# Performance work log

Measured on AMD Instinct MI355X. Metric: run time of the kernel, lower is better.

## Reference

```python
import jax, jax.numpy as jnp
import numpy as np

B, H, M, HS = 256, 1024, 256, 128  # batch, hidden=entry_size, mem_cap, head_size
TAU = 1.0
sg = jax.lax.stop_gradient


def _gumbel(u):
    # torch: -log(1e-20 - log(1e-20 + rand))
    return -jnp.log(1e-20 - jnp.log(1e-20 + u))


def _hard_gumbel_softmax(scores, u, tau):
    # straight-through hard gumbel softmax over the memcap axis (axis=1)
    y = jax.nn.softmax((scores + sg(_gumbel(u))) * tau, axis=1)
    ymax = jnp.max(y, axis=1, keepdims=True)
    hard = (y == ymax).astype(y.dtype)
    return sg(hard - y) + y


def setup_inputs() -> dict:
    key = jax.random.key(0)
    ks = jax.random.split(key, 20)
    stdv = 1.0 / np.sqrt(H)
    U = lambda k, shp: jax.random.uniform(k, shp, jnp.float32, -stdv, stdv)
    inp = {
        'input_': jax.random.normal(ks[0], (B, H), jnp.float32),
        'h_0': jax.random.normal(ks[1], (B, H), jnp.float32),
        'mem': jnp.zeros((B, M, H), jnp.float32),
        'last_usage': jnp.full((B, M), -99999.0, jnp.float32),
        'u1': jax.random.uniform(ks[2], (B, M), jnp.float32),
        'u2': jax.random.uniform(ks[3], (B, M), jnp.float32),
        'W_ih': U(ks[4], (H, 3 * H)),
        'W_hh': U(ks[5], (H, 3 * H)),
        'W_rh': U(ks[6], (H, 3 * H)),
        'W_s1': U(ks[7], (H, H)),
        'W_s2': U(ks[8], (H, H)),
        'W_s3': U(ks[9], (H, H)),
        'bias': jnp.zeros((1, 3 * H), jnp.float32),
        'W_im': U(ks[10], (H, HS + 1)),
        'W_hm': U(ks[11], (H, HS + 1)),
        'fc1_w': U(ks[12], (HS, H)),
        'fc1_b': jnp.zeros((HS,), jnp.float32),
        'W_im1': U(ks[13], (H, HS + 1)),
        'W_hm1': U(ks[14], (H, HS + 1)),
        'W_mm1': U(ks[15], (H, HS + 1)),
        'bias_m1': jnp.zeros((1, HS + 1), jnp.float32),
        'bias_1': jnp.zeros((1, H), jnp.float32),
        'bias_2': jnp.zeros((1, H), jnp.float32),
        'bias_3': jnp.zeros((1, H), jnp.float32),
    }
    return inp


def reference(input_, h_0, mem, last_usage, u1, u2,
              W_ih, W_hh, W_rh, W_s1, W_s2, W_s3, bias,
              W_im, W_hm, fc1_w, fc1_b,
              W_im1, W_hm1, W_mm1, bias_m1, bias_1, bias_2, bias_3):
    memcap = mem.shape[1]
    hidden = h_0.shape[1]
    # write: memcnt == 0 -> one-hot write index at slot 0, broadcast over batch
    widx = jnp.zeros((1, memcap), mem.dtype).at[0, 0].set(1.0)
    ones = widx[:, :, None]                       # (1, M, 1)
    mem = h_0[:, None, :] * ones + mem * (1.0 - ones)  # (B, M, E)
    last_use = jax.nn.sigmoid(sg(last_usage))     # (B, M), detached
    # addressing head (computed on detached input/h_0/mem, as in torch)
    read_head = jnp.tanh(sg(input_) @ W_im + sg(h_0) @ W_hm)          # (B, HS+1)
    head_vecs = jnp.concatenate(
        [sg(mem) @ fc1_w.T + fc1_b, last_use[:, :, None]], axis=2)    # (B, M, HS+1)
    scores = jnp.einsum('bh,bmh->bm', read_head, head_vecs)
    y1 = _hard_gumbel_softmax(scores, u1, TAU)
    entry = jnp.einsum('bm,bme->be', y1, mem)     # (B, E)
    # GRU-like gating
    w_b = jax.nn.sigmoid(entry @ W_rh + h_0 @ W_hh + input_ @ W_ih + bias)
    r, z, n = jnp.split(w_b, 3, axis=1)
    h_new = jnp.tanh(input_ @ W_s1 + bias_1 + r * (h_0 @ W_s2 + bias_2)
                     + z * (bias_3 + entry @ W_s3))
    # second read head (not detached)
    head1 = jnp.tanh(input_ @ W_im1 + h_0 @ W_hm1 + entry @ W_mm1 + bias_m1)
    scores1 = jnp.einsum('bh,bmh->bm', head1, head_vecs)
    y2 = _hard_gumbel_softmax(scores1, u2, TAU)
    entry_o = jnp.einsum('bm,bme->be', y2, mem)
    h_1 = n * h_new + (1.0 - n) * h_0
    o = jnp.concatenate([h_1, entry_o], axis=1)
    return (h_1, o)
```

## Files before the change

### kernel.cpp

```cpp
#include <hip/hip_runtime.h>

#define BB 256
#define HH 1024
#define MM 256
#define HS 128
#define NH 129

typedef __attribute__((ext_vector_type(8))) short short8;
typedef __attribute__((ext_vector_type(4))) float float4v;

__device__ __forceinline__ float sigmoidf_(float x) { return 1.0f / (1.0f + expf(-x)); }
__device__ __forceinline__ float gumbelf_(float u) { return -logf(1e-20f - logf(1e-20f + u)); }

__device__ __forceinline__ unsigned short f2bf(float x) {
    union { float f; unsigned u; } c; c.f = x;
    unsigned u = c.u;
    return (unsigned short)((u + 0x7FFFu + ((u >> 16) & 1u)) >> 16);
}

__global__ __launch_bounds__(256) void k_heads_project(const float* __restrict__ input_,
                                                       const float* __restrict__ h0,
                                                       const float* __restrict__ W_im,
                                                       const float* __restrict__ W_hm,
                                                       const float* __restrict__ fc1_w,
                                                       const float* __restrict__ fc1_b,
                                                       float* __restrict__ read_head,
                                                       float* __restrict__ v,
                                                       float* __restrict__ c) {
    __shared__ float sx[HH], sh[HH];
    __shared__ float sj[NH];
    int b = blockIdx.x, t = threadIdx.x;
    for (int i = t; i < HH / 4; i += 256) {
        ((float4*)sx)[i] = ((const float4*)(input_ + (size_t)b * HH))[i];
        ((float4*)sh)[i] = ((const float4*)(h0 + (size_t)b * HH))[i];
    }
    __syncthreads();
    if (t < NH) {
        float acc = 0.f;
#pragma unroll 8
        for (int h = 0; h < HH; ++h)
            acc += sx[h] * W_im[h * NH + t] + sh[h] * W_hm[h * NH + t];
        float tv = tanhf(acc);
        read_head[b * NH + t] = tv;
        sj[t] = tv;
    }
    __syncthreads();
    {
        int hb = t * 4;
        float4 a = make_float4(0.f, 0.f, 0.f, 0.f);
#pragma unroll 4
        for (int j = 0; j < HS; ++j) {
            float s = sj[j];
            float4 w = *(const float4*)(fc1_w + (size_t)j * HH + hb);
            a.x += s * w.x; a.y += s * w.y; a.z += s * w.z; a.w += s * w.w;
        }
        *(float4*)(v + (size_t)b * HH + hb) = a;
    }
    if (t == 0) {
        float acc = 0.f;
        for (int j = 0; j < HS; ++j) acc += sj[j] * fc1_b[j];
        c[b] = acc;
    }
}

__global__ __launch_bounds__(256) void k_scores(const float* __restrict__ mem,
                                                const float* __restrict__ h0,
                                                const float* __restrict__ v,
                                                const float* __restrict__ c,
                                                const float* __restrict__ head,
                                                const float* __restrict__ last_usage,
                                                const float* __restrict__ u,
                                                float* __restrict__ sg_out) {
    int b = blockIdx.x;
    int wave = threadIdx.x >> 6, lane = threadIdx.x & 63;
    int mstart = blockIdx.y * 32 + wave * 8;
    float4 rv[4];
#pragma unroll
    for (int it = 0; it < 4; ++it)
        rv[it] = *(const float4*)(v + (size_t)b * HH + it * 256 + lane * 4);
    float cb = c[b];
    float hf = head[b * NH + HS];
    for (int i = 0; i < 8; ++i) {
        int m = mstart + i;
        const float* row = (m == 0) ? (h0 + (size_t)b * HH) : (mem + ((size_t)(b * MM + m)) * HH);
        float p = 0.f;
#pragma unroll
        for (int it = 0; it < 4; ++it) {
            float4 mv = *(const float4*)(row + it * 256 + lane * 4);
            p += mv.x * rv[it].x + mv.y * rv[it].y + mv.z * rv[it].z + mv.w * rv[it].w;
        }
        for (int off = 32; off > 0; off >>= 1) p += __shfl_down(p, off, 64);
        if (lane == 0) {
            float lu = sigmoidf_(last_usage[b * MM + m]);
            sg_out[b * MM + m] = p + cb + hf * lu + gumbelf_(u[b * MM + m]);
        }
    }
}

__global__ __launch_bounds__(256) void k_sel1(const float* __restrict__ sg1,
                                              const float* __restrict__ mem,
                                              const float* __restrict__ h0,
                                              const float* __restrict__ input_,
                                              const float* __restrict__ W_im1,
                                              const float* __restrict__ W_hm1,
                                              const float* __restrict__ W_mm1,
                                              const float* __restrict__ bias_m1,
                                              const float* __restrict__ fc1_w,
                                              const float* __restrict__ fc1_b,
                                              float* __restrict__ entry,
                                              float* __restrict__ head1,
                                              float* __restrict__ v2,
                                              float* __restrict__ c2) {
    __shared__ float svals[256];
    __shared__ int sidx[256];
    __shared__ float se[HH], sx[HH], sh[HH];
    __shared__ float sj[NH];
    int b = blockIdx.x, t = threadIdx.x;
    svals[t] = sg1[b * MM + t];
    sidx[t] = t;
    __syncthreads();
    for (int s = 128; s > 0; s >>= 1) {
        if (t < s) {
            if (svals[t + s] > svals[t]) { svals[t] = svals[t + s]; sidx[t] = sidx[t + s]; }
        }
        __syncthreads();
    }
    int mstar = sidx[0];
    const float* row = (mstar == 0) ? (h0 + (size_t)b * HH) : (mem + ((size_t)(b * MM + mstar)) * HH);
    {
        int hb = t * 4;
        float4 e = *(const float4*)(row + hb);
        *(float4*)(se + hb) = e;
        *(float4*)(entry + (size_t)b * HH + hb) = e;
        *(float4*)(sx + hb) = *(const float4*)(input_ + (size_t)b * HH + hb);
        *(float4*)(sh + hb) = *(const float4*)(h0 + (size_t)b * HH + hb);
    }
    __syncthreads();
    if (t < NH) {
        float acc = bias_m1[t];
#pragma unroll 8
        for (int h = 0; h < HH; ++h)
            acc += sx[h] * W_im1[h * NH + t] + sh[h] * W_hm1[h * NH + t] + se[h] * W_mm1[h * NH + t];
        float hv = tanhf(acc);
        head1[b * NH + t] = hv;
        sj[t] = hv;
    }
    __syncthreads();
    {
        int hb = t * 4;
        float4 a = make_float4(0.f, 0.f, 0.f, 0.f);
#pragma unroll 4
        for (int j = 0; j < HS; ++j) {
            float s = sj[j];
            float4 w = *(const float4*)(fc1_w + (size_t)j * HH + hb);
            a.x += s * w.x; a.y += s * w.y; a.z += s * w.z; a.w += s * w.w;
        }
        *(float4*)(v2 + (size_t)b * HH + hb) = a;
    }
    if (t == 0) {
        float acc = 0.f;
        for (int j = 0; j < HS; ++j) acc += sj[j] * fc1_b[j];
        c2[b] = acc;
    }
}

__global__ __launch_bounds__(256) void k_cvt_act(const float* __restrict__ input_,
                                                 const float* __restrict__ h0,
                                                 const float* __restrict__ entry,
                                                 unsigned short* __restrict__ Abf) {
    int idx = blockIdx.x * 256 + threadIdx.x;
    int e0 = idx * 4;
    int m = e0 / 3072;
    int kk = e0 - m * 3072;
    int seg = kk >> 10, kin = kk & 1023;
    const float* src = (seg == 0 ? input_ : seg == 1 ? h0 : entry) + m * 1024 + kin;
    float4 v = *(const float4*)src;
    ushort4 o;
    o.x = f2bf(v.x); o.y = f2bf(v.y); o.z = f2bf(v.z); o.w = f2bf(v.w);
    *(ushort4*)(Abf + e0) = o;
}

__global__ __launch_bounds__(256) void k_cvt_w(const float* __restrict__ W_ih,
                                               const float* __restrict__ W_hh,
                                               const float* __restrict__ W_rh,
                                               const float* __restrict__ W_s1,
                                               const float* __restrict__ W_s2,
                                               const float* __restrict__ W_s3,
                                               unsigned short* __restrict__ WtG,
                                               unsigned short* __restrict__ WtS) {
    __shared__ unsigned short T[64][66];
    int bx = blockIdx.x;
    const float* src;
    unsigned short* dst;
    int k0, n0, sstr, dstr, krel;
    if (bx < 2304) {
        int kt = bx / 48, nt = bx % 48;
        k0 = kt * 64; n0 = nt * 64;
        src = (k0 < 1024) ? W_ih : (k0 < 2048) ? W_hh : W_rh;
        krel = k0 & 1023;
        dst = WtG; sstr = 3072; dstr = 3072;
    } else {
        int r = bx - 2304;
        int seg = r >> 8;
        int rem = r & 255;
        int kt = rem >> 4, nt = rem & 15;
        k0 = kt * 64; n0 = nt * 64;
        src = (seg == 0) ? W_s1 : (seg == 1) ? W_s2 : W_s3;
        krel = k0;
        dst = WtS + (size_t)seg * 1048576; sstr = 1024; dstr = 1024;
    }
    int t = threadIdx.x;
    for (int i = 0; i < 16; ++i) {
        int e = i * 256 + t;
        int kk = e >> 6, nn = e & 63;
        T[nn][kk] = f2bf(src[(size_t)(krel + kk) * sstr + n0 + nn]);
    }
    __syncthreads();
    for (int i = 0; i < 8; ++i) {
        int e = i * 256 + t;
        int nn = e >> 5, kk2 = (e & 31) * 2;
        unsigned val = (unsigned)T[nn][kk2] | ((unsigned)T[nn][kk2 + 1] << 16);
        *(unsigned*)(dst + (size_t)(n0 + nn) * dstr + k0 + kk2) = val;
    }
}

__global__ __launch_bounds__(256) void k_gemm(const unsigned short* __restrict__ Abf,
                                              const unsigned short* __restrict__ WtG,
                                              const unsigned short* __restrict__ WtS,
                                              float* __restrict__ wbp,
                                              float* __restrict__ S) {
    __shared__ unsigned short As[128 * 72];
    __shared__ unsigned short Bs[128 * 72];
    int bx = blockIdx.x;
    int mtile = bx & 1, unit = bx >> 1;
    int m0 = mtile * 128;
    const unsigned short* Bp;
    int bstr, ksel, ncol0;
    bool iswb;
    if (unit < 72) {
        iswb = true;
        int nt = unit % 24;
        ksel = unit / 24;
        ncol0 = nt * 128;
        Bp = WtG + (size_t)ncol0 * 3072 + ksel * 1024;
        bstr = 3072;
    } else {
        iswb = false;
        int su = unit - 72;
        int seg = su >> 3, nts = su & 7;
        ksel = seg;
        ncol0 = seg * 1024 + nts * 128;
        Bp = WtS + (size_t)seg * 1048576 + (size_t)(nts * 128) * 1024;
        bstr = 1024;
    }
    const unsigned short* Ap = Abf + ksel * 1024;

    int tid = threadIdx.x;
    int wave = tid >> 6, lane = tid & 63;
    int wm = wave >> 1, wn = wave & 1;
    int q = lane >> 4, lm = lane & 15;

    float4v acc[4][4];
    for (int i = 0; i < 4; ++i)
        for (int j = 0; j < 4; ++j)
            acc[i][j] = (float4v){0.f, 0.f, 0.f, 0.f};

    for (int kt = 0; kt < 1024; kt += 64) {
        for (int rr = 0; rr < 4; ++rr) {
            int e = rr * 256 + tid;
            int row = e >> 3, cg = e & 7;
            *(uint4*)&As[row * 72 + cg * 8] =
                *(const uint4*)(Ap + (size_t)(m0 + row) * 3072 + kt + cg * 8);
            *(uint4*)&Bs[row * 72 + cg * 8] =
                *(const uint4*)(Bp + (size_t)row * bstr + kt + cg * 8);
        }
        __syncthreads();
        for (int ks = 0; ks < 64; ks += 32) {
            short8 av[4], bv[4];
            for (int i = 0; i < 4; ++i)
                av[i] = *(const short8*)&As[(wm * 64 + i * 16 + lm) * 72 + ks + q * 8];
            for (int j = 0; j < 4; ++j)
                bv[j] = *(const short8*)&Bs[(wn * 64 + j * 16 + lm) * 72 + ks + q * 8];
            for (int i = 0; i < 4; ++i)
                for (int j = 0; j < 4; ++j)
                    acc[i][j] = __builtin_amdgcn_mfma_f32_16x16x32_bf16(av[i], bv[j], acc[i][j], 0, 0, 0);
        }
        __syncthreads();
    }

    for (int i = 0; i < 4; ++i)
        for (int j = 0; j < 4; ++j) {
            int n = ncol0 + wn * 64 + j * 16 + lm;
            for (int reg = 0; reg < 4; ++reg) {
                int m = m0 + wm * 64 + i * 16 + q * 4 + reg;
                float val = acc[i][j][reg];
                if (iswb) wbp[(size_t)ksel * 786432 + (size_t)m * 3072 + n] = val;
                else S[(size_t)m * 3072 + n] = val;
            }
        }
}

__global__ __launch_bounds__(256) void k_final(const float* __restrict__ sg2,
                                               const float* __restrict__ mem,
                                               const float* __restrict__ wbp,
                                               const float* __restrict__ S,
                                               const float* __restrict__ h0,
                                               const float* __restrict__ bias,
                                               const float* __restrict__ b1,
                                               const float* __restrict__ b2,
                                               const float* __restrict__ b3,
                                               float* __restrict__ out) {
    __shared__ float svals[256];
    __shared__ int sidx[256];
    int b = blockIdx.x, t = threadIdx.x;
    svals[t] = sg2[b * MM + t];
    sidx[t] = t;
    __syncthreads();
    for (int s = 128; s > 0; s >>= 1) {
        if (t < s) {
            if (svals[t + s] > svals[t]) { svals[t] = svals[t + s]; sidx[t] = sidx[t + s]; }
        }
        __syncthreads();
    }
    int mstar = sidx[0];
    const float* erow = (mstar == 0) ? (h0 + (size_t)b * HH) : (mem + ((size_t)(b * MM + mstar)) * HH);
    float* o_row = out + (size_t)BB * HH + (size_t)b * 2 * HH;
    {
        int hb = t * 4;
        *(float4*)(o_row + HH + hb) = *(const float4*)(erow + hb);
    }
    int h = t * 4;
    const float* p0 = wbp + (size_t)b * 3072;
    const float* p1 = wbp + 786432 + (size_t)b * 3072;
    const float* p2 = wbp + 2 * 786432 + (size_t)b * 3072;
    const float* Sp = S + (size_t)b * 3072;
    float4 w0 = *(const float4*)(p0 + h);
    float4 w1 = *(const float4*)(p1 + h);
    float4 w2 = *(const float4*)(p2 + h);
    float4 bi = *(const float4*)(bias + h);
    float4 r4 = make_float4(sigmoidf_(w0.x + w1.x + w2.x + bi.x), sigmoidf_(w0.y + w1.y + w2.y + bi.y),
                            sigmoidf_(w0.z + w1.z + w2.z + bi.z), sigmoidf_(w0.w + w1.w + w2.w + bi.w));
    w0 = *(const float4*)(p0 + 1024 + h);
    w1 = *(const float4*)(p1 + 1024 + h);
    w2 = *(const float4*)(p2 + 1024 + h);
    bi = *(const float4*)(bias + 1024 + h);
    float4 z4 = make_float4(sigmoidf_(w0.x + w1.x + w2.x + bi.x), sigmoidf_(w0.y + w1.y + w2.y + bi.y),
                            sigmoidf_(w0.z + w1.z + w2.z + bi.z), sigmoidf_(w0.w + w1.w + w2.w + bi.w));
    w0 = *(const float4*)(p0 + 2048 + h);
    w1 = *(const float4*)(p1 + 2048 + h);
    w2 = *(const float4*)(p2 + 2048 + h);
    bi = *(const float4*)(bias + 2048 + h);
    float4 n4 = make_float4(sigmoidf_(w0.x + w1.x + w2.x + bi.x), sigmoidf_(w0.y + w1.y + w2.y + bi.y),
                            sigmoidf_(w0.z + w1.z + w2.z + bi.z), sigmoidf_(w0.w + w1.w + w2.w + bi.w));
    float4 s1 = *(const float4*)(Sp + h);
    float4 s2 = *(const float4*)(Sp + 1024 + h);
    float4 s3 = *(const float4*)(Sp + 2048 + h);
    float4 v1 = *(const float4*)(b1 + h);
    float4 v2 = *(const float4*)(b2 + h);
    float4 v3 = *(const float4*)(b3 + h);
    float4 h0v = *(const float4*)(h0 + (size_t)b * HH + h);
    float4 hn, h1;
    hn.x = tanhf(s1.x + v1.x + r4.x * (s2.x + v2.x) + z4.x * (s3.x + v3.x));
    hn.y = tanhf(s1.y + v1.y + r4.y * (s2.y + v2.y) + z4.y * (s3.y + v3.y));
    hn.z = tanhf(s1.z + v1.z + r4.z * (s2.z + v2.z) + z4.z * (s3.z + v3.z));
    hn.w = tanhf(s1.w + v1.w + r4.w * (s2.w + v2.w) + z4.w * (s3.w + v3.w));
    h1.x = n4.x * hn.x + (1.f - n4.x) * h0v.x;
    h1.y = n4.y * hn.y + (1.f - n4.y) * h0v.y;
    h1.z = n4.z * hn.z + (1.f - n4.z) * h0v.z;
    h1.w = n4.w * hn.w + (1.f - n4.w) * h0v.w;
    *(float4*)(out + (size_t)b * HH + h) = h1;
    *(float4*)(o_row + h) = h1;
}

extern "C" void kernel_launch(void* const* d_in, const int* in_sizes, int n_in,
                              void* d_out, int out_size, void* d_ws, size_t ws_size,
                              hipStream_t stream) {
    const float* input_ = (const float*)d_in[0];
    const float* h0 = (const float*)d_in[1];
    const float* mem = (const float*)d_in[2];
    const float* last_usage = (const float*)d_in[3];
    const float* u1 = (const float*)d_in[4];
    const float* u2 = (const float*)d_in[5];
    const float* W_ih = (const float*)d_in[6];
    const float* W_hh = (const float*)d_in[7];
    const float* W_rh = (const float*)d_in[8];
    const float* W_s1 = (const float*)d_in[9];
    const float* W_s2 = (const float*)d_in[10];
    const float* W_s3 = (const float*)d_in[11];
    const float* bias = (const float*)d_in[12];
    const float* W_im = (const float*)d_in[13];
    const float* W_hm = (const float*)d_in[14];
    const float* fc1_w = (const float*)d_in[15];
    const float* fc1_b = (const float*)d_in[16];
    const float* W_im1 = (const float*)d_in[17];
    const float* W_hm1 = (const float*)d_in[18];
    const float* W_mm1 = (const float*)d_in[19];
    const float* bias_m1 = (const float*)d_in[20];
    const float* bias_1 = (const float*)d_in[21];
    const float* bias_2 = (const float*)d_in[22];
    const float* bias_3 = (const float*)d_in[23];
    float* out = (float*)d_out;

    float* ws = (float*)d_ws;
    float* read_head = ws;
    float* head1 = read_head + 33024;
    float* v1 = head1 + 33024;
    float* v2 = v1 + 262144;
    float* c1 = v2 + 262144;
    float* c2 = c1 + 256;
    float* sg1 = c2 + 256;
    float* sg2 = sg1 + 65536;
    float* entry = sg2 + 65536;
    float* wbp = entry + 262144;
    float* S = wbp + 3 * 786432;
    unsigned short* Abf = (unsigned short*)(S + 786432);
    unsigned short* WtG = Abf + 786432;
    unsigned short* WtS = WtG + 9437184;

    k_cvt_w<<<3072, 256, 0, stream>>>(W_ih, W_hh, W_rh, W_s1, W_s2, W_s3, WtG, WtS);
    k_heads_project<<<BB, 256, 0, stream>>>(input_, h0, W_im, W_hm, fc1_w, fc1_b, read_head, v1, c1);
    k_scores<<<dim3(BB, 8), 256, 0, stream>>>(mem, h0, v1, c1, read_head, last_usage, u1, sg1);
    k_sel1<<<BB, 256, 0, stream>>>(sg1, mem, h0, input_, W_im1, W_hm1, W_mm1, bias_m1,
                                   fc1_w, fc1_b, entry, head1, v2, c2);
    k_cvt_act<<<768, 256, 0, stream>>>(input_, h0, entry, Abf);
    k_scores<<<dim3(BB, 8), 256, 0, stream>>>(mem, h0, v2, c2, head1, last_usage, u2, sg2);
    k_gemm<<<192, 256, 0, stream>>>(Abf, WtG, WtS, wbp, S);
    k_final<<<BB, 256, 0, stream>>>(sg2, mem, wbp, S, h0, bias, bias_1, bias_2, bias_3, out);
}
```

Before: 701.9 us.

## Fuse head projection and scoring kernels, split GEMM K dimension, vectorize weight conversion

Merges the head projection, score computation and activation bf16 conversion into two 1024-thread kernels, one per read head, so the v/c/head intermediates stay in shared memory and four launches go away. The head projection splits its K loop across 8 thread groups to use more threads. The GEMM is split in K halves, doubling the grid to 384 blocks for better CU occupancy, and k_final sums the partial results. The weight transpose conversion uses float4 loads. The cost is extra partial-sum traffic and reduced parallelism in the scoring phase, with 256 blocks each covering a whole batch row.

```diff
diff --git a/kernel.cpp b/kernel.cpp
--- a/kernel.cpp
+++ b/kernel.cpp
@@ -16,168 +16,6 @@
     union { float f; unsigned u; } c; c.f = x;
     unsigned u = c.u;
     return (unsigned short)((u + 0x7FFFu + ((u >> 16) & 1u)) >> 16);
-}
-
-__global__ __launch_bounds__(256) void k_heads_project(const float* __restrict__ input_,
-                                                       const float* __restrict__ h0,
-                                                       const float* __restrict__ W_im,
-                                                       const float* __restrict__ W_hm,
-                                                       const float* __restrict__ fc1_w,
-                                                       const float* __restrict__ fc1_b,
-                                                       float* __restrict__ read_head,
-                                                       float* __restrict__ v,
-                                                       float* __restrict__ c) {
-    __shared__ float sx[HH], sh[HH];
-    __shared__ float sj[NH];
-    int b = blockIdx.x, t = threadIdx.x;
-    for (int i = t; i < HH / 4; i += 256) {
-        ((float4*)sx)[i] = ((const float4*)(input_ + (size_t)b * HH))[i];
-        ((float4*)sh)[i] = ((const float4*)(h0 + (size_t)b * HH))[i];
-    }
-    __syncthreads();
-    if (t < NH) {
-        float acc = 0.f;
-#pragma unroll 8
-        for (int h = 0; h < HH; ++h)
-            acc += sx[h] * W_im[h * NH + t] + sh[h] * W_hm[h * NH + t];
-        float tv = tanhf(acc);
-        read_head[b * NH + t] = tv;
-        sj[t] = tv;
-    }
-    __syncthreads();
-    {
-        int hb = t * 4;
-        float4 a = make_float4(0.f, 0.f, 0.f, 0.f);
-#pragma unroll 4
-        for (int j = 0; j < HS; ++j) {
-            float s = sj[j];
-            float4 w = *(const float4*)(fc1_w + (size_t)j * HH + hb);
-            a.x += s * w.x; a.y += s * w.y; a.z += s * w.z; a.w += s * w.w;
-        }
-        *(float4*)(v + (size_t)b * HH + hb) = a;
-    }
-    if (t == 0) {
-        float acc = 0.f;
-        for (int j = 0; j < HS; ++j) acc += sj[j] * fc1_b[j];
-        c[b] = acc;
-    }
-}
-
-__global__ __launch_bounds__(256) void k_scores(const float* __restrict__ mem,
-                                                const float* __restrict__ h0,
-                                                const float* __restrict__ v,
-                                                const float* __restrict__ c,
-                                                const float* __restrict__ head,
-                                                const float* __restrict__ last_usage,
-                                                const float* __restrict__ u,
-                                                float* __restrict__ sg_out) {
-    int b = blockIdx.x;
-    int wave = threadIdx.x >> 6, lane = threadIdx.x & 63;
-    int mstart = blockIdx.y * 32 + wave * 8;
-    float4 rv[4];
-#pragma unroll
-    for (int it = 0; it < 4; ++it)
-        rv[it] = *(const float4*)(v + (size_t)b * HH + it * 256 + lane * 4);
-    float cb = c[b];
-    float hf = head[b * NH + HS];
-    for (int i = 0; i < 8; ++i) {
-        int m = mstart + i;
-        const float* row = (m == 0) ? (h0 + (size_t)b * HH) : (mem + ((size_t)(b * MM + m)) * HH);
-        float p = 0.f;
-#pragma unroll
-        for (int it = 0; it < 4; ++it) {
-            float4 mv = *(const float4*)(row + it * 256 + lane * 4);
-            p += mv.x * rv[it].x + mv.y * rv[it].y + mv.z * rv[it].z + mv.w * rv[it].w;
-        }
-        for (int off = 32; off > 0; off >>= 1) p += __shfl_down(p, off, 64);
-        if (lane == 0) {
-            float lu = sigmoidf_(last_usage[b * MM + m]);
-            sg_out[b * MM + m] = p + cb + hf * lu + gumbelf_(u[b * MM + m]);
-        }
-    }
-}
-
-__global__ __launch_bounds__(256) void k_sel1(const float* __restrict__ sg1,
-                                              const float* __restrict__ mem,
-                                              const float* __restrict__ h0,
-                                              const float* __restrict__ input_,
-                                              const float* __restrict__ W_im1,
-                                              const float* __restrict__ W_hm1,
-                                              const float* __restrict__ W_mm1,
-                                              const float* __restrict__ bias_m1,
-                                              const float* __restrict__ fc1_w,
-                                              const float* __restrict__ fc1_b,
-                                              float* __restrict__ entry,
-                                              float* __restrict__ head1,
-                                              float* __restrict__ v2,
-                                              float* __restrict__ c2) {
-    __shared__ float svals[256];
-    __shared__ int sidx[256];
-    __shared__ float se[HH], sx[HH], sh[HH];
-    __shared__ float sj[NH];
-    int b = blockIdx.x, t = threadIdx.x;
-    svals[t] = sg1[b * MM + t];
-    sidx[t] = t;
-    __syncthreads();
-    for (int s = 128; s > 0; s >>= 1) {
-        if (t < s) {
-            if (svals[t + s] > svals[t]) { svals[t] = svals[t + s]; sidx[t] = sidx[t + s]; }
-        }
-        __syncthreads();
-    }
-    int mstar = sidx[0];
-    const float* row = (mstar == 0) ? (h0 + (size_t)b * HH) : (mem + ((size_t)(b * MM + mstar)) * HH);
-    {
-        int hb = t * 4;
-        float4 e = *(const float4*)(row + hb);
-        *(float4*)(se + hb) = e;
-        *(float4*)(entry + (size_t)b * HH + hb) = e;
-        *(float4*)(sx + hb) = *(const float4*)(input_ + (size_t)b * HH + hb);
-        *(float4*)(sh + hb) = *(const float4*)(h0 + (size_t)b * HH + hb);
-    }
-    __syncthreads();
-    if (t < NH) {
-        float acc = bias_m1[t];
-#pragma unroll 8
-        for (int h = 0; h < HH; ++h)
-            acc += sx[h] * W_im1[h * NH + t] + sh[h] * W_hm1[h * NH + t] + se[h] * W_mm1[h * NH + t];
-        float hv = tanhf(acc);
-        head1[b * NH + t] = hv;
-        sj[t] = hv;
-    }
-    __syncthreads();
-    {
-        int hb = t * 4;
-        float4 a = make_float4(0.f, 0.f, 0.f, 0.f);
-#pragma unroll 4
-        for (int j = 0; j < HS; ++j) {
-            float s = sj[j];
-            float4 w = *(const float4*)(fc1_w + (size_t)j * HH + hb);
-            a.x += s * w.x; a.y += s * w.y; a.z += s * w.z; a.w += s * w.w;
-        }
-        *(float4*)(v2 + (size_t)b * HH + hb) = a;
-    }
-    if (t == 0) {
-        float acc = 0.f;
-        for (int j = 0; j < HS; ++j) acc += sj[j] * fc1_b[j];
-        c2[b] = acc;
-    }
-}
-
-__global__ __launch_bounds__(256) void k_cvt_act(const float* __restrict__ input_,
-                                                 const float* __restrict__ h0,
-                                                 const float* __restrict__ entry,
-                                                 unsigned short* __restrict__ Abf) {
-    int idx = blockIdx.x * 256 + threadIdx.x;
-    int e0 = idx * 4;
-    int m = e0 / 3072;
-    int kk = e0 - m * 3072;
-    int seg = kk >> 10, kin = kk & 1023;
-    const float* src = (seg == 0 ? input_ : seg == 1 ? h0 : entry) + m * 1024 + kin;
-    float4 v = *(const float4*)src;
-    ushort4 o;
-    o.x = f2bf(v.x); o.y = f2bf(v.y); o.z = f2bf(v.z); o.w = f2bf(v.w);
-    *(ushort4*)(Abf + e0) = o;
 }
 
 __global__ __launch_bounds__(256) void k_cvt_w(const float* __restrict__ W_ih,
@@ -210,10 +48,14 @@
         dst = WtS + (size_t)seg * 1048576; sstr = 1024; dstr = 1024;
     }
     int t = threadIdx.x;
-    for (int i = 0; i < 16; ++i) {
+    for (int i = 0; i < 4; ++i) {
         int e = i * 256 + t;
-        int kk = e >> 6, nn = e & 63;
-        T[nn][kk] = f2bf(src[(size_t)(krel + kk) * sstr + n0 + nn]);
+        int kk = e >> 4, nn0 = (e & 15) * 4;
+        float4 v = *(const float4*)(src + (size_t)(krel + kk) * sstr + n0 + nn0);
+        T[nn0 + 0][kk] = f2bf(v.x);
+        T[nn0 + 1][kk] = f2bf(v.y);
+        T[nn0 + 2][kk] = f2bf(v.z);
+        T[nn0 + 3][kk] = f2bf(v.w);
     }
     __syncthreads();
     for (int i = 0; i < 8; ++i) {
@@ -224,36 +66,244 @@
     }
 }
 
+__global__ __launch_bounds__(1024) void k_score1(const float* __restrict__ input_,
+                                                 const float* __restrict__ h0,
+                                                 const float* __restrict__ W_im,
+                                                 const float* __restrict__ W_hm,
+                                                 const float* __restrict__ fc1_w,
+                                                 const float* __restrict__ fc1_b,
+                                                 const float* __restrict__ mem,
+                                                 const float* __restrict__ last_usage,
+                                                 const float* __restrict__ u1,
+                                                 unsigned short* __restrict__ Abf,
+                                                 float* __restrict__ sg_out) {
+    __shared__ float sx[HH], sh[HH], sv[HH];
+    __shared__ float red[8][128];
+    __shared__ float red2[8];
+    __shared__ float sj[NH];
+    __shared__ float scb;
+    int b = blockIdx.x, t = threadIdx.x;
+    if (t < 256) {
+        float4 v = *(const float4*)(input_ + (size_t)b * HH + t * 4);
+        *(float4*)(sx + t * 4) = v;
+        ushort4 o; o.x = f2bf(v.x); o.y = f2bf(v.y); o.z = f2bf(v.z); o.w = f2bf(v.w);
+        *(ushort4*)(Abf + (size_t)b * 3072 + t * 4) = o;
+    } else if (t < 512) {
+        int tt = t - 256;
+        float4 v = *(const float4*)(h0 + (size_t)b * HH + tt * 4);
+        *(float4*)(sh + tt * 4) = v;
+        ushort4 o; o.x = f2bf(v.x); o.y = f2bf(v.y); o.z = f2bf(v.z); o.w = f2bf(v.w);
+        *(ushort4*)(Abf + (size_t)b * 3072 + 1024 + tt * 4) = o;
+    }
+    __syncthreads();
+    {
+        int j = t & 127, ks = t >> 7;
+        int hb = ks * 128;
+        float p = 0.f;
+#pragma unroll 8
+        for (int h = hb; h < hb + 128; ++h)
+            p += sx[h] * W_im[h * NH + j] + sh[h] * W_hm[h * NH + j];
+        red[ks][j] = p;
+        if (t >= 1016) {
+            int k2 = t - 1016;
+            int hb2 = k2 * 128;
+            float q = 0.f;
+#pragma unroll 8
+            for (int h = hb2; h < hb2 + 128; ++h)
+                q += sx[h] * W_im[h * NH + 128] + sh[h] * W_hm[h * NH + 128];
+            red2[k2] = q;
+        }
+    }
+    __syncthreads();
+    if (t < 128) {
+        float s = 0.f;
+        for (int k = 0; k < 8; ++k) s += red[k][t];
+        sj[t] = tanhf(s);
+    } else if (t == 128) {
+        float s = 0.f;
+        for (int k = 0; k < 8; ++k) s += red2[k];
+        sj[128] = tanhf(s);
+    }
+    __syncthreads();
+    {
+        float acc = 0.f;
+#pragma unroll 4
+        for (int j = 0; j < HS; ++j) acc += sj[j] * fc1_w[(size_t)j * HH + t];
+        sv[t] = acc;
+    }
+    if (t < 64) {
+        float p = sj[t] * fc1_b[t] + sj[t + 64] * fc1_b[t + 64];
+        for (int off = 32; off > 0; off >>= 1) p += __shfl_down(p, off, 64);
+        if (t == 0) scb = p;
+    }
+    __syncthreads();
+    float cb = scb, hf = sj[128];
+    int wave = t >> 6, lane = t & 63;
+    float4 rv[4];
+#pragma unroll
+    for (int it = 0; it < 4; ++it) rv[it] = *(const float4*)(sv + it * 256 + lane * 4);
+    for (int i = 0; i < 16; ++i) {
+        int m = wave * 16 + i;
+        const float* row = (m == 0) ? (h0 + (size_t)b * HH) : (mem + ((size_t)(b * MM + m)) * HH);
+        float p = 0.f;
+#pragma unroll
+        for (int it = 0; it < 4; ++it) {
+            float4 mv = *(const float4*)(row + it * 256 + lane * 4);
+            p += mv.x * rv[it].x + mv.y * rv[it].y + mv.z * rv[it].z + mv.w * rv[it].w;
+        }
+        for (int off = 32; off > 0; off >>= 1) p += __shfl_down(p, off, 64);
+        if (lane == 0) {
+            float lu = sigmoidf_(last_usage[b * MM + m]);
+            sg_out[b * MM + m] = p + cb + hf * lu + gumbelf_(u1[b * MM + m]);
+        }
+    }
+}
+
+__global__ __launch_bounds__(1024) void k_sel_score2(const float* __restrict__ sg1,
+                                                     const float* __restrict__ mem,
+                                                     const float* __restrict__ h0,
+                                                     const float* __restrict__ input_,
+                                                     const float* __restrict__ W_im1,
+                                                     const float* __restrict__ W_hm1,
+                                                     const float* __restrict__ W_mm1,
+                                                     const float* __restrict__ bias_m1,
+                                                     const float* __restrict__ fc1_w,
+                                                     const float* __restrict__ fc1_b,
+                                                     const float* __restrict__ last_usage,
+                                                     const float* __restrict__ u2,
+                                                     unsigned short* __restrict__ Abf,
+                                                     float* __restrict__ sg_out) {
+    __shared__ float svals[256];
+    __shared__ int sidx[256];
+    __shared__ float sx[HH], sh[HH], se[HH], sv[HH];
+    __shared__ float red[8][128];
+    __shared__ float red2[8];
+    __shared__ float sj[NH];
+    __shared__ float scb;
+    int b = blockIdx.x, t = threadIdx.x;
+    if (t < 256) {
+        svals[t] = sg1[b * MM + t];
+        sidx[t] = t;
+    }
+    __syncthreads();
+    for (int s = 128; s > 0; s >>= 1) {
+        if (t < s) {
+            if (svals[t + s] > svals[t]) { svals[t] = svals[t + s]; sidx[t] = sidx[t + s]; }
+        }
+        __syncthreads();
+    }
+    int mstar = sidx[0];
+    const float* erow = (mstar == 0) ? (h0 + (size_t)b * HH) : (mem + ((size_t)(b * MM + mstar)) * HH);
+    if (t < 256) {
+        float4 v = *(const float4*)(erow + t * 4);
+        *(float4*)(se + t * 4) = v;
+        ushort4 o; o.x = f2bf(v.x); o.y = f2bf(v.y); o.z = f2bf(v.z); o.w = f2bf(v.w);
+        *(ushort4*)(Abf + (size_t)b * 3072 + 2048 + t * 4) = o;
+    } else if (t < 512) {
+        int tt = t - 256;
+        *(float4*)(sx + tt * 4) = *(const float4*)(input_ + (size_t)b * HH + tt * 4);
+    } else if (t < 768) {
+        int tt = t - 512;
+        *(float4*)(sh + tt * 4) = *(const float4*)(h0 + (size_t)b * HH + tt * 4);
+    }
+    __syncthreads();
+    {
+        int j = t & 127, ks = t >> 7;
+        int hb = ks * 128;
+        float p = 0.f;
+#pragma unroll 4
+        for (int h = hb; h < hb + 128; ++h)
+            p += sx[h] * W_im1[h * NH + j] + sh[h] * W_hm1[h * NH + j] + se[h] * W_mm1[h * NH + j];
+        red[ks][j] = p;
+        if (t >= 1016) {
+            int k2 = t - 1016;
+            int hb2 = k2 * 128;
+            float q = 0.f;
+#pragma unroll 4
+            for (int h = hb2; h < hb2 + 128; ++h)
+                q += sx[h] * W_im1[h * NH + 128] + sh[h] * W_hm1[h * NH + 128] + se[h] * W_mm1[h * NH + 128];
+            red2[k2] = q;
+        }
+    }
+    __syncthreads();
+    if (t < 128) {
+        float s = bias_m1[t];
+        for (int k = 0; k < 8; ++k) s += red[k][t];
+        sj[t] = tanhf(s);
+    } else if (t == 128) {
+        float s = bias_m1[128];
+        for (int k = 0; k < 8; ++k) s += red2[k];
+        sj[128] = tanhf(s);
+    }
+    __syncthreads();
+    {
+        float acc = 0.f;
+#pragma unroll 4
+        for (int j = 0; j < HS; ++j) acc += sj[j] * fc1_w[(size_t)j * HH + t];
+        sv[t] = acc;
+    }
+    if (t < 64) {
+        float p = sj[t] * fc1_b[t] + sj[t + 64] * fc1_b[t + 64];
+        for (int off = 32; off > 0; off >>= 1) p += __shfl_down(p, off, 64);
+        if (t == 0) scb = p;
+    }
+    __syncthreads();
+    float cb = scb, hf = sj[128];
+    int wave = t >> 6, lane = t & 63;
+    float4 rv[4];
+#pragma unroll
+    for (int it = 0; it < 4; ++it) rv[it] = *(const float4*)(sv + it * 256 + lane * 4);
+    for (int i = 0; i < 16; ++i) {
+        int m = wave * 16 + i;
+        const float* row = (m == 0) ? (h0 + (size_t)b * HH) : (mem + ((size_t)(b * MM + m)) * HH);
+        float p = 0.f;
+#pragma unroll
+        for (int it = 0; it < 4; ++it) {
+            float4 mv = *(const float4*)(row + it * 256 + lane * 4);
+            p += mv.x * rv[it].x + mv.y * rv[it].y + mv.z * rv[it].z + mv.w * rv[it].w;
+        }
+        for (int off = 32; off > 0; off >>= 1) p += __shfl_down(p, off, 64);
+        if (lane == 0) {
+            float lu = sigmoidf_(last_usage[b * MM + m]);
+            sg_out[b * MM + m] = p + cb + hf * lu + gumbelf_(u2[b * MM + m]);
+        }
+    }
+}
+
 __global__ __launch_bounds__(256) void k_gemm(const unsigned short* __restrict__ Abf,
                                               const unsigned short* __restrict__ WtG,
                                               const unsigned short* __restrict__ WtS,
                                               float* __restrict__ wbp,
-                                              float* __restrict__ S) {
+                                              float* __restrict__ Sp) {
     __shared__ unsigned short As[128 * 72];
     __shared__ unsigned short Bs[128 * 72];
     int bx = blockIdx.x;
     int mtile = bx & 1, unit = bx >> 1;
     int m0 = mtile * 128;
     const unsigned short* Bp;
-    int bstr, ksel, ncol0;
-    bool iswb;
-    if (unit < 72) {
-        iswb = true;
+    const unsigned short* Ap;
+    float* pout;
+    int bstr, ncol0;
+    if (unit < 144) {
         int nt = unit % 24;
-        ksel = unit / 24;
+        int kidx = unit / 24;
+        int ksel = kidx >> 1, khalf = kidx & 1;
         ncol0 = nt * 128;
-        Bp = WtG + (size_t)ncol0 * 3072 + ksel * 1024;
+        Bp = WtG + (size_t)ncol0 * 3072 + ksel * 1024 + khalf * 512;
         bstr = 3072;
+        Ap = Abf + ksel * 1024 + khalf * 512;
+        pout = wbp + (size_t)kidx * 786432;
     } else {
-        iswb = false;
-        int su = unit - 72;
-        int seg = su >> 3, nts = su & 7;
-        ksel = seg;
+        int su = unit - 144;
+        int seg = su / 16;
+        int rem = su % 16;
+        int khalf = rem >> 3, nts = rem & 7;
         ncol0 = seg * 1024 + nts * 128;
-        Bp = WtS + (size_t)seg * 1048576 + (size_t)(nts * 128) * 1024;
+        Bp = WtS + (size_t)seg * 1048576 + (size_t)(nts * 128) * 1024 + khalf * 512;
         bstr = 1024;
-    }
-    const unsigned short* Ap = Abf + ksel * 1024;
+        Ap = Abf + seg * 1024 + khalf * 512;
+        pout = Sp + (size_t)khalf * 786432;
+    }
 
     int tid = threadIdx.x;
     int wave = tid >> 6, lane = tid & 63;
@@ -265,7 +315,7 @@
         for (int j = 0; j < 4; ++j)
             acc[i][j] = (float4v){0.f, 0.f, 0.f, 0.f};
 
-    for (int kt = 0; kt < 1024; kt += 64) {
+    for (int kt = 0; kt < 512; kt += 64) {
         for (int rr = 0; rr < 4; ++rr) {
             int e = rr * 256 + tid;
             int row = e >> 3, cg = e & 7;
@@ -293,9 +343,7 @@
             int n = ncol0 + wn * 64 + j * 16 + lm;
             for (int reg = 0; reg < 4; ++reg) {
                 int m = m0 + wm * 64 + i * 16 + q * 4 + reg;
-                float val = acc[i][j][reg];
-                if (iswb) wbp[(size_t)ksel * 786432 + (size_t)m * 3072 + n] = val;
-                else S[(size_t)m * 3072 + n] = val;
+                pout[(size_t)m * 3072 + n] = acc[i][j][reg];
             }
         }
 }
@@ -303,7 +351,7 @@
 __global__ __launch_bounds__(256) void k_final(const float* __restrict__ sg2,
                                                const float* __restrict__ mem,
                                                const float* __restrict__ wbp,
-                                               const float* __restrict__ S,
+                                               const float* __restrict__ Sp,
                                                const float* __restrict__ h0,
                                                const float* __restrict__ bias,
                                                const float* __restrict__ b1,
@@ -330,31 +378,39 @@
         *(float4*)(o_row + HH + hb) = *(const float4*)(erow + hb);
     }
     int h = t * 4;
-    const float* p0 = wbp + (size_t)b * 3072;
-    const float* p1 = wbp + 786432 + (size_t)b * 3072;
-    const float* p2 = wbp + 2 * 786432 + (size_t)b * 3072;
-    const float* Sp = S + (size_t)b * 3072;
-    float4 w0 = *(const float4*)(p0 + h);
-    float4 w1 = *(const float4*)(p1 + h);
-    float4 w2 = *(const float4*)(p2 + h);
-    float4 bi = *(const float4*)(bias + h);
-    float4 r4 = make_float4(sigmoidf_(w0.x + w1.x + w2.x + bi.x), sigmoidf_(w0.y + w1.y + w2.y + bi.y),
-                            sigmoidf_(w0.z + w1.z + w2.z + bi.z), sigmoidf_(w0.w + w1.w + w2.w + bi.w));
-    w0 = *(const float4*)(p0 + 1024 + h);
-    w1 = *(const float4*)(p1 + 1024 + h);
-    w2 = *(const float4*)(p2 + 1024 + h);
-    bi = *(const float4*)(bias + 1024 + h);
-    float4 z4 = make_float4(sigmoidf_(w0.x + w1.x + w2.x + bi.x), sigmoidf_(w0.y + w1.y + w2.y + bi.y),
-                            sigmoidf_(w0.z + w1.z + w2.z + bi.z), sigmoidf_(w0.w + w1.w + w2.w + bi.w));
-    w0 = *(const float4*)(p0 + 2048 + h);
-    w1 = *(const float4*)(p1 + 2048 + h);
-    w2 = *(const float4*)(p2 + 2048 + h);
-    bi = *(const float4*)(bias + 2048 + h);
-    float4 n4 = make_float4(sigmoidf_(w0.x + w1.x + w2.x + bi.x), sigmoidf_(w0.y + w1.y + w2.y + bi.y),
-                            sigmoidf_(w0.z + w1.z + w2.z + bi.z), sigmoidf_(w0.w + w1.w + w2.w + bi.w));
-    float4 s1 = *(const float4*)(Sp + h);
-    float4 s2 = *(const float4*)(Sp + 1024 + h);
-    float4 s3 = *(const float4*)(Sp + 2048 + h);
+    size_t base = (size_t)b * 3072;
+    float4 wsum[3];
+#pragma unroll
+    for (int g = 0; g < 3; ++g) {
+        float4 a = make_float4(0.f, 0.f, 0.f, 0.f);
+#pragma unroll
+        for (int p = 0; p < 6; ++p) {
+            float4 w = *(const float4*)(wbp + (size_t)p * 786432 + base + g * 1024 + h);
+            a.x += w.x; a.y += w.y; a.z += w.z; a.w += w.w;
+        }
+        wsum[g] = a;
+    }
+    float4 bi0 = *(const float4*)(bias + h);
+    float4 bi1 = *(const float4*)(bias + 1024 + h);
+    float4 bi2 = *(const float4*)(bias + 2048 + h);
+    float4 r4 = make_float4(sigmoidf_(wsum[0].x + bi0.x), sigmoidf_(wsum[0].y + bi0.y),
+                            sigmoidf_(wsum[0].z + bi0.z), sigmoidf_(wsum[0].w + bi0.w));
+    float4 z4 = make_float4(sigmoidf_(wsum[1].x + bi1.x), sigmoidf_(wsum[1].y + bi1.y),
+                            sigmoidf_(wsum[1].z + bi1.z), sigmoidf_(wsum[1].w + bi1.w));
+    float4 n4 = make_float4(sigmoidf_(wsum[2].x + bi2.x), sigmoidf_(wsum[2].y + bi2.y),
+                            sigmoidf_(wsum[2].z + bi2.z), sigmoidf_(wsum[2].w + bi2.w));
+    float4 s1, s2, s3;
+    {
+        float4 a0 = *(const float4*)(Sp + base + h);
+        float4 a1 = *(const float4*)(Sp + 786432 + base + h);
+        s1 = make_float4(a0.x + a1.x, a0.y + a1.y, a0.z + a1.z, a0.w + a1.w);
+        a0 = *(const float4*)(Sp + base + 1024 + h);
+        a1 = *(const float4*)(Sp + 786432 + base + 1024 + h);
+        s2 = make_float4(a0.x + a1.x, a0.y + a1.y, a0.z + a1.z, a0.w + a1.w);
+        a0 = *(const float4*)(Sp + base + 2048 + h);
+        a1 = *(const float4*)(Sp + 786432 + base + 2048 + h);
+        s3 = make_float4(a0.x + a1.x, a0.y + a1.y, a0.z + a1.z, a0.w + a1.w);
+    }
     float4 v1 = *(const float4*)(b1 + h);
     float4 v2 = *(const float4*)(b2 + h);
     float4 v3 = *(const float4*)(b3 + h);
@@ -402,28 +458,19 @@
     float* out = (float*)d_out;
 
     float* ws = (float*)d_ws;
-    float* read_head = ws;
-    float* head1 = read_head + 33024;
-    float* v1 = head1 + 33024;
-    float* v2 = v1 + 262144;
-    float* c1 = v2 + 262144;
-    float* c2 = c1 + 256;
-    float* sg1 = c2 + 256;
+    float* sg1 = ws;
     float* sg2 = sg1 + 65536;
-    float* entry = sg2 + 65536;
-    float* wbp = entry + 262144;
-    float* S = wbp + 3 * 786432;
-    unsigned short* Abf = (unsigned short*)(S + 786432);
+    float* wbp = sg2 + 65536;
+    float* Sp = wbp + 6 * 786432;
+    unsigned short* Abf = (unsigned short*)(Sp + 2 * 786432);
     unsigned short* WtG = Abf + 786432;
     unsigned short* WtS = WtG + 9437184;
 
     k_cvt_w<<<3072, 256, 0, stream>>>(W_ih, W_hh, W_rh, W_s1, W_s2, W_s3, WtG, WtS);
-    k_heads_project<<<BB, 256, 0, stream>>>(input_, h0, W_im, W_hm, fc1_w, fc1_b, read_head, v1, c1);
-    k_scores<<<dim3(BB, 8), 256, 0, stream>>>(mem, h0, v1, c1, read_head, last_usage, u1, sg1);
-    k_sel1<<<BB, 256, 0, stream>>>(sg1, mem, h0, input_, W_im1, W_hm1, W_mm1, bias_m1,
-                                   fc1_w, fc1_b, entry, head1, v2, c2);
-    k_cvt_act<<<768, 256, 0, stream>>>(input_, h0, entry, Abf);
-    k_scores<<<dim3(BB, 8), 256, 0, stream>>>(mem, h0, v2, c2, head1, last_usage, u2, sg2);
-    k_gemm<<<192, 256, 0, stream>>>(Abf, WtG, WtS, wbp, S);
-    k_final<<<BB, 256, 0, stream>>>(sg2, mem, wbp, S, h0, bias, bias_1, bias_2, bias_3, out);
-}
+    k_score1<<<BB, 1024, 0, stream>>>(input_, h0, W_im, W_hm, fc1_w, fc1_b,
+                                      mem, last_usage, u1, Abf, sg1);
+    k_sel_score2<<<BB, 1024, 0, stream>>>(sg1, mem, h0, input_, W_im1, W_hm1, W_mm1, bias_m1,
+                                          fc1_w, fc1_b, last_usage, u2, Abf, sg2);
+    k_gemm<<<384, 256, 0, stream>>>(Abf, WtG, WtS, wbp, Sp);
+    k_final<<<BB, 256, 0, stream>>>(sg2, mem, wbp, Sp, h0, bias, bias_1, bias_2, bias_3, out);
+}
```

Measured after the change: 595.9 us. 1.18x faster.
